# Performance work log

Hardware: AMD Instinct MI355X
Metric: run time of the kernel (lower is better)

Reference implementation:

```python
import jax, jax.numpy as jnp
import numpy as np

B, T, F, U = 64, 512, 1024, 64


def setup_inputs() -> dict:
    key = jax.random.key(0)
    ks = jax.random.split(key, 6)
    return {
        "x": jax.random.normal(ks[0], (B, T, F), dtype=jnp.float32),
        "kernel": jax.random.normal(ks[1], (F, U), dtype=jnp.float32) * (1.0 / np.sqrt(F)),
        "bias": jax.random.normal(ks[2], (U,), dtype=jnp.float32) * 0.02,
        "chain_kernel": jax.random.normal(ks[3], (U, U), dtype=jnp.float32) * 0.1,
        "left_boundary": jax.random.normal(ks[4], (U,), dtype=jnp.float32) * 0.1,
        "right_boundary": jax.random.normal(ks[5], (U,), dtype=jnp.float32) * 0.1,
    }


def _viterbi_decode(potentials, chain_kernel):
    # potentials: [B, T, U], chain_kernel: [U, U]
    def step(alpha, pot_t):
        # alpha: [B, U] best score ending in each tag at t-1
        scores = alpha[:, :, None] + chain_kernel[None, :, :] + pot_t[:, None, :]  # [B, U_prev, U_cur]
        return jnp.max(scores, axis=1), jnp.argmax(scores, axis=1)

    pots_t = jnp.moveaxis(potentials[:, 1:], 1, 0)  # [T-1, B, U]
    alpha_last, backptrs = jax.lax.scan(step, potentials[:, 0], pots_t)
    last_tag = jnp.argmax(alpha_last, axis=-1)  # [B]

    def back(tag, bp):
        prev = jnp.take_along_axis(bp, tag[:, None], axis=1)[:, 0]
        return prev, prev

    _, tags = jax.lax.scan(back, last_tag, backptrs, reverse=True)  # [T-1, B], positions 0..T-2
    path = jnp.concatenate([jnp.moveaxis(tags, 0, 1), last_tag[:, None]], axis=1)
    return path.astype(jnp.int32)


def reference(x, kernel, bias, chain_kernel, left_boundary, right_boundary):
    # dense projection (activation = linear)
    potentials = jnp.einsum("btf,fu->btu", x, kernel) + bias  # [B, T, U]
    # boundary energies (mask=None path: add to first/last timestep)
    potentials = potentials.at[:, 0, :].add(left_boundary)
    potentials = potentials.at[:, -1, :].add(right_boundary)
    return _viterbi_decode(potentials, chain_kernel)
```

## Files before the change

kernel.cpp:

```cpp
#include <hip/hip_runtime.h>

#define B_ 64
#define T_ 512
#define F_ 1024
#define U_ 64
#define FK 128
#define NCH (F_ / FK)

__device__ __forceinline__ void block_barrier_lds() {
    asm volatile("s_waitcnt lgkmcnt(0)" ::: "memory");
    __builtin_amdgcn_s_barrier();
    asm volatile("" ::: "memory");
}

__global__ __launch_bounds__(256, 2) void crf_gemm_kernel(
    const float* __restrict__ x, const float* __restrict__ w,
    const float* __restrict__ bias, const float* __restrict__ lb,
    const float* __restrict__ rb, float* __restrict__ pot)
{
    __shared__ float wlds[FK * U_];

    const int tid = threadIdx.x;
    const int rt = tid >> 4;
    const int ut = tid & 15;
    const int n0 = blockIdx.x * 64;
    const int r0 = rt * 4;
    const int u0 = ut * 4;

    float acc[4][4];
#pragma unroll
    for (int i = 0; i < 4; ++i)
#pragma unroll
        for (int j = 0; j < 4; ++j) acc[i][j] = 0.f;

    const float* xrow = x + (size_t)(n0 + r0) * F_;

    float4 wst[8];
#pragma unroll
    for (int l = 0; l < 8; ++l)
        wst[l] = *reinterpret_cast<const float4*>(w + (size_t)(l * 256 + tid) * 4);
#pragma unroll
    for (int l = 0; l < 8; ++l)
        *reinterpret_cast<float4*>(&wlds[(l * 256 + tid) * 4]) = wst[l];
    __syncthreads();

    float4 xp0[4], xp1[4];
#pragma unroll
    for (int i = 0; i < 4; ++i)
        xp0[i] = *reinterpret_cast<const float4*>(xrow + (size_t)i * F_ + 0);
#pragma unroll
    for (int i = 0; i < 4; ++i)
        xp1[i] = *reinterpret_cast<const float4*>(xrow + (size_t)i * F_ + 4);

    for (int c = 0; c < NCH; ++c) {
        if (c + 1 < NCH) {
#pragma unroll
            for (int l = 0; l < 8; ++l)
                wst[l] = *reinterpret_cast<const float4*>(
                    w + (size_t)(c + 1) * (FK * U_) + (size_t)(l * 256 + tid) * 4);
        }

        float4 wc[4];
#pragma unroll
        for (int j = 0; j < 4; ++j)
            wc[j] = *reinterpret_cast<const float4*>(&wlds[(0 + j) * U_ + u0]);

        for (int kk = 0; kk < FK / 4; ++kk) {
            const int kg = (c * FK + kk * 4 + 8) & (F_ - 1);
            float4 xn[4];
#pragma unroll
            for (int i = 0; i < 4; ++i)
                xn[i] = *reinterpret_cast<const float4*>(xrow + (size_t)i * F_ + kg);

            float4 wn[4];
            const int krn = (kk * 4 + 4) & (FK - 1);
#pragma unroll
            for (int j = 0; j < 4; ++j)
                wn[j] = *reinterpret_cast<const float4*>(&wlds[(krn + j) * U_ + u0]);

#pragma unroll
            for (int ff = 0; ff < 4; ++ff) {
                const float4 wf = wc[ff];
#pragma unroll
                for (int i = 0; i < 4; ++i) {
                    const float xs = (ff == 0) ? xp0[i].x : (ff == 1) ? xp0[i].y
                                   : (ff == 2) ? xp0[i].z : xp0[i].w;
                    acc[i][0] = fmaf(xs, wf.x, acc[i][0]);
                    acc[i][1] = fmaf(xs, wf.y, acc[i][1]);
                    acc[i][2] = fmaf(xs, wf.z, acc[i][2]);
                    acc[i][3] = fmaf(xs, wf.w, acc[i][3]);
                }
            }
#pragma unroll
            for (int i = 0; i < 4; ++i) { xp0[i] = xp1[i]; xp1[i] = xn[i]; }
#pragma unroll
            for (int j = 0; j < 4; ++j) wc[j] = wn[j];
        }

        if (c + 1 < NCH) {
            __syncthreads();
#pragma unroll
            for (int l = 0; l < 8; ++l)
                *reinterpret_cast<float4*>(&wlds[(l * 256 + tid) * 4]) = wst[l];
            __syncthreads();
        }
    }

    const int t0 = n0 & (T_ - 1);
    const float4 bs4 = *reinterpret_cast<const float4*>(bias + u0);
    const float4 lb4 = *reinterpret_cast<const float4*>(lb + u0);
    const float4 rb4 = *reinterpret_cast<const float4*>(rb + u0);

#pragma unroll
    for (int i = 0; i < 4; ++i) {
        const int n = n0 + r0 + i;
        const int t = t0 + r0 + i;
        float4 o;
        o.x = acc[i][0] + bs4.x;
        o.y = acc[i][1] + bs4.y;
        o.z = acc[i][2] + bs4.z;
        o.w = acc[i][3] + bs4.w;
        if (t == 0)      { o.x += lb4.x; o.y += lb4.y; o.z += lb4.z; o.w += lb4.w; }
        if (t == T_ - 1) { o.x += rb4.x; o.y += rb4.y; o.z += rb4.z; o.w += rb4.w; }
        *reinterpret_cast<float4*>(pot + (size_t)n * U_ + u0) = o;
    }
}

__global__ __launch_bounds__(256) void crf_viterbi_kernel(
    const float* __restrict__ pot, const float* __restrict__ chain,
    int* __restrict__ path)
{
    const int b = blockIdx.x;
    const int tid = threadIdx.x;
    const int u = tid & 63;
    const int g = tid >> 6;

    __shared__ __align__(16) float alpha_s[64];
    __shared__ float pval[4][64];
    __shared__ int   pidx[4][64];
    __shared__ unsigned char bp[T_ - 1][64];
    __shared__ unsigned char cmap[4][64];
    __shared__ int es[4];

    float chain_r[16];
#pragma unroll
    for (int k = 0; k < 16; ++k)
        chain_r[k] = chain[(size_t)(g * 16 + k) * U_ + u];

    const float* potb = pot + (size_t)b * T_ * U_;

    if (g == 0) alpha_s[u] = potb[u];

    float p0 = potb[1 * U_ + u];
    float p1 = potb[2 * U_ + u];
    float p2 = potb[3 * U_ + u];
    block_barrier_lds();

    for (int t = 1; t < T_; ++t) {
        const int tp = (t + 3 < T_) ? (t + 3) : (T_ - 1);
        const float pnew = potb[(size_t)tp * U_ + u];
        const float pc = p0;

        const float4* a4 = reinterpret_cast<const float4*>(alpha_s);
        float s[16];
#pragma unroll
        for (int q = 0; q < 4; ++q) {
            const float4 av = a4[g * 4 + q];
            s[q * 4 + 0] = (av.x + chain_r[q * 4 + 0]) + pc;
            s[q * 4 + 1] = (av.y + chain_r[q * 4 + 1]) + pc;
            s[q * 4 + 2] = (av.z + chain_r[q * 4 + 2]) + pc;
            s[q * 4 + 3] = (av.w + chain_r[q * 4 + 3]) + pc;
        }
        float tv[8]; int ti[8];
#pragma unroll
        for (int i = 0; i < 8; ++i) {
            const bool gt = s[2 * i + 1] > s[2 * i];
            tv[i] = gt ? s[2 * i + 1] : s[2 * i];
            ti[i] = gt ? 2 * i + 1 : 2 * i;
        }
        float uv[4]; int ui[4];
#pragma unroll
        for (int i = 0; i < 4; ++i) {
            const bool gt = tv[2 * i + 1] > tv[2 * i];
            uv[i] = gt ? tv[2 * i + 1] : tv[2 * i];
            ui[i] = gt ? ti[2 * i + 1] : ti[2 * i];
        }
        const bool g0_ = uv[1] > uv[0];
        const float w0 = g0_ ? uv[1] : uv[0];
        const int   i0 = g0_ ? ui[1] : ui[0];
        const bool g1_ = uv[3] > uv[2];
        const float w1 = g1_ ? uv[3] : uv[2];
        const int   i1 = g1_ ? ui[3] : ui[2];
        const bool gf = w1 > w0;
        const float bv16 = gf ? w1 : w0;
        const int   bi16 = gf ? i1 : i0;

        pval[g][u] = bv16;
        pidx[g][u] = g * 16 + bi16;
        block_barrier_lds();

        if (g == 0) {
            float bv = pval[0][u];
            int   bi = pidx[0][u];
#pragma unroll
            for (int j = 1; j < 4; ++j) {
                const float vv = pval[j][u];
                if (vv > bv) { bv = vv; bi = pidx[j][u]; }
            }
            alpha_s[u] = bv;
            bp[t - 1][u] = (unsigned char)bi;
        }
        block_barrier_lds();

        p0 = p1; p1 = p2; p2 = pnew;
    }

    const int r0c = g * 128;
    const int r1c = (g == 3) ? (T_ - 1) : (g + 1) * 128;

    {
        int tag = u;
        for (int r = r1c - 1; r >= r0c; --r) tag = bp[r][tag];
        cmap[g][u] = (unsigned char)tag;
    }
    block_barrier_lds();

    if (tid == 0) {
        float bvv = alpha_s[0];
        int bii = 0;
        for (int v = 1; v < 64; ++v) {
            const float a = alpha_s[v];
            if (a > bvv) { bvv = a; bii = v; }
        }
        path[(size_t)b * T_ + (T_ - 1)] = bii;
        const int e3 = bii;
        const int e2 = cmap[3][e3];
        const int e1 = cmap[2][e2];
        const int e0 = cmap[1][e1];
        es[0] = e0; es[1] = e1; es[2] = e2; es[3] = e3;
    }
    block_barrier_lds();

    if (u == 0) {
        int tag = es[g];
        int* pb = path + (size_t)b * T_;
        for (int r = r1c - 1; r >= r0c; --r) {
            tag = bp[r][tag];
            pb[r] = tag;
        }
    }
}

extern "C" void kernel_launch(void* const* d_in, const int* in_sizes, int n_in,
                              void* d_out, int out_size, void* d_ws, size_t ws_size,
                              hipStream_t stream) {
    const float* x  = (const float*)d_in[0];
    const float* w  = (const float*)d_in[1];
    const float* bs = (const float*)d_in[2];
    const float* ck = (const float*)d_in[3];
    const float* lb = (const float*)d_in[4];
    const float* rb = (const float*)d_in[5];

    float* pot = (float*)d_ws;
    int* path  = (int*)d_out;

    crf_gemm_kernel<<<dim3(B_ * T_ / 64), dim3(256), 0, stream>>>(x, w, bs, lb, rb, pot);
    crf_viterbi_kernel<<<dim3(B_), dim3(256), 0, stream>>>(pot, ck, path);
}
```

Baseline: 413.9 us.

## Halve GEMM row tile, raise occupancy, simplify Viterbi argmax and barriers

The GEMM kernel now gives each block 32 rows instead of 64, each thread 2 rows instead of 4, and launch bounds target 4 blocks per CU, doubling the grid. The goal is more parallelism and occupancy on the memory-bound projection, at the cost of reloading the weight matrix into LDS twice as often. The Viterbi kernel swaps its tree-reduction argmax for a sequential scan and its custom LDS barrier for __syncthreads, and prefetches one timestep ahead instead of three. That lengthens the serial dependency chain and exposes more global-load latency in the latency-bound recurrence.

```diff
diff --git a/kernel.cpp b/kernel.cpp
--- a/kernel.cpp
+++ b/kernel.cpp
@@ -7,13 +7,7 @@
 #define FK 128
 #define NCH (F_ / FK)
 
-__device__ __forceinline__ void block_barrier_lds() {
-    asm volatile("s_waitcnt lgkmcnt(0)" ::: "memory");
-    __builtin_amdgcn_s_barrier();
-    asm volatile("" ::: "memory");
-}
-
-__global__ __launch_bounds__(256, 2) void crf_gemm_kernel(
+__global__ __launch_bounds__(256, 4) void crf_gemm_kernel(
     const float* __restrict__ x, const float* __restrict__ w,
     const float* __restrict__ bias, const float* __restrict__ lb,
     const float* __restrict__ rb, float* __restrict__ pot)
@@ -23,13 +17,13 @@
     const int tid = threadIdx.x;
     const int rt = tid >> 4;
     const int ut = tid & 15;
-    const int n0 = blockIdx.x * 64;
-    const int r0 = rt * 4;
+    const int n0 = blockIdx.x * 32;
+    const int r0 = rt * 2;
     const int u0 = ut * 4;
 
-    float acc[4][4];
-#pragma unroll
-    for (int i = 0; i < 4; ++i)
+    float acc[2][4];
+#pragma unroll
+    for (int i = 0; i < 2; ++i)
 #pragma unroll
         for (int j = 0; j < 4; ++j) acc[i][j] = 0.f;
 
@@ -44,12 +38,12 @@
         *reinterpret_cast<float4*>(&wlds[(l * 256 + tid) * 4]) = wst[l];
     __syncthreads();
 
-    float4 xp0[4], xp1[4];
-#pragma unroll
-    for (int i = 0; i < 4; ++i)
+    float4 xp0[2], xp1[2];
+#pragma unroll
+    for (int i = 0; i < 2; ++i)
         xp0[i] = *reinterpret_cast<const float4*>(xrow + (size_t)i * F_ + 0);
 #pragma unroll
-    for (int i = 0; i < 4; ++i)
+    for (int i = 0; i < 2; ++i)
         xp1[i] = *reinterpret_cast<const float4*>(xrow + (size_t)i * F_ + 4);
 
     for (int c = 0; c < NCH; ++c) {
@@ -67,9 +61,9 @@
 
         for (int kk = 0; kk < FK / 4; ++kk) {
             const int kg = (c * FK + kk * 4 + 8) & (F_ - 1);
-            float4 xn[4];
-#pragma unroll
-            for (int i = 0; i < 4; ++i)
+            float4 xn[2];
+#pragma unroll
+            for (int i = 0; i < 2; ++i)
                 xn[i] = *reinterpret_cast<const float4*>(xrow + (size_t)i * F_ + kg);
 
             float4 wn[4];
@@ -82,7 +76,7 @@
             for (int ff = 0; ff < 4; ++ff) {
                 const float4 wf = wc[ff];
 #pragma unroll
-                for (int i = 0; i < 4; ++i) {
+                for (int i = 0; i < 2; ++i) {
                     const float xs = (ff == 0) ? xp0[i].x : (ff == 1) ? xp0[i].y
                                    : (ff == 2) ? xp0[i].z : xp0[i].w;
                     acc[i][0] = fmaf(xs, wf.x, acc[i][0]);
@@ -92,7 +86,7 @@
                 }
             }
 #pragma unroll
-            for (int i = 0; i < 4; ++i) { xp0[i] = xp1[i]; xp1[i] = xn[i]; }
+            for (int i = 0; i < 2; ++i) { xp0[i] = xp1[i]; xp1[i] = xn[i]; }
 #pragma unroll
             for (int j = 0; j < 4; ++j) wc[j] = wn[j];
         }
@@ -112,7 +106,7 @@
     const float4 rb4 = *reinterpret_cast<const float4*>(rb + u0);
 
 #pragma unroll
-    for (int i = 0; i < 4; ++i) {
+    for (int i = 0; i < 2; ++i) {
         const int n = n0 + r0 + i;
         const int t = t0 + r0 + i;
         float4 o;
@@ -150,69 +144,44 @@
     const float* potb = pot + (size_t)b * T_ * U_;
 
     if (g == 0) alpha_s[u] = potb[u];
-
-    float p0 = potb[1 * U_ + u];
-    float p1 = potb[2 * U_ + u];
-    float p2 = potb[3 * U_ + u];
-    block_barrier_lds();
+    __syncthreads();
+
+    float pc = potb[(size_t)U_ + u];
 
     for (int t = 1; t < T_; ++t) {
-        const int tp = (t + 3 < T_) ? (t + 3) : (T_ - 1);
-        const float pnew = potb[(size_t)tp * U_ + u];
-        const float pc = p0;
+        const int tn = (t + 1 < T_) ? (t + 1) : (T_ - 1);
+        const float pn = potb[(size_t)tn * U_ + u];
 
         const float4* a4 = reinterpret_cast<const float4*>(alpha_s);
-        float s[16];
+        float best = -3.402823466e38f;
+        int bidx = 0;
 #pragma unroll
         for (int q = 0; q < 4; ++q) {
             const float4 av = a4[g * 4 + q];
-            s[q * 4 + 0] = (av.x + chain_r[q * 4 + 0]) + pc;
-            s[q * 4 + 1] = (av.y + chain_r[q * 4 + 1]) + pc;
-            s[q * 4 + 2] = (av.z + chain_r[q * 4 + 2]) + pc;
-            s[q * 4 + 3] = (av.w + chain_r[q * 4 + 3]) + pc;
-        }
-        float tv[8]; int ti[8];
-#pragma unroll
-        for (int i = 0; i < 8; ++i) {
-            const bool gt = s[2 * i + 1] > s[2 * i];
-            tv[i] = gt ? s[2 * i + 1] : s[2 * i];
-            ti[i] = gt ? 2 * i + 1 : 2 * i;
-        }
-        float uv[4]; int ui[4];
-#pragma unroll
-        for (int i = 0; i < 4; ++i) {
-            const bool gt = tv[2 * i + 1] > tv[2 * i];
-            uv[i] = gt ? tv[2 * i + 1] : tv[2 * i];
-            ui[i] = gt ? ti[2 * i + 1] : ti[2 * i];
-        }
-        const bool g0_ = uv[1] > uv[0];
-        const float w0 = g0_ ? uv[1] : uv[0];
-        const int   i0 = g0_ ? ui[1] : ui[0];
-        const bool g1_ = uv[3] > uv[2];
-        const float w1 = g1_ ? uv[3] : uv[2];
-        const int   i1 = g1_ ? ui[3] : ui[2];
-        const bool gf = w1 > w0;
-        const float bv16 = gf ? w1 : w0;
-        const int   bi16 = gf ? i1 : i0;
-
-        pval[g][u] = bv16;
-        pidx[g][u] = g * 16 + bi16;
-        block_barrier_lds();
-
+            const float avv[4] = {av.x, av.y, av.z, av.w};
+#pragma unroll
+            for (int kk = 0; kk < 4; ++kk) {
+                const int k = q * 4 + kk;
+                const float s2 = (avv[kk] + chain_r[k]) + pc;
+                if (s2 > best) { best = s2; bidx = g * 16 + k; }
+            }
+        }
+        pval[g][u] = best;
+        pidx[g][u] = bidx;
+        __syncthreads();
         if (g == 0) {
             float bv = pval[0][u];
             int   bi = pidx[0][u];
 #pragma unroll
             for (int j = 1; j < 4; ++j) {
-                const float vv = pval[j][u];
-                if (vv > bv) { bv = vv; bi = pidx[j][u]; }
+                const float v = pval[j][u];
+                if (v > bv) { bv = v; bi = pidx[j][u]; }
             }
+            bp[t - 1][u] = (unsigned char)bi;
             alpha_s[u] = bv;
-            bp[t - 1][u] = (unsigned char)bi;
-        }
-        block_barrier_lds();
-
-        p0 = p1; p1 = p2; p2 = pnew;
+        }
+        __syncthreads();
+        pc = pn;
     }
 
     const int r0c = g * 128;
@@ -223,7 +192,7 @@
         for (int r = r1c - 1; r >= r0c; --r) tag = bp[r][tag];
         cmap[g][u] = (unsigned char)tag;
     }
-    block_barrier_lds();
+    __syncthreads();
 
     if (tid == 0) {
         float bvv = alpha_s[0];
@@ -239,7 +208,7 @@
         const int e0 = cmap[1][e1];
         es[0] = e0; es[1] = e1; es[2] = e2; es[3] = e3;
     }
-    block_barrier_lds();
+    __syncthreads();
 
     if (u == 0) {
         int tag = es[g];
@@ -264,6 +233,6 @@
     float* pot = (float*)d_ws;
     int* path  = (int*)d_out;
 
-    crf_gemm_kernel<<<dim3(B_ * T_ / 64), dim3(256), 0, stream>>>(x, w, bs, lb, rb, pot);
+    crf_gemm_kernel<<<dim3(B_ * T_ / 32), dim3(256), 0, stream>>>(x, w, bs, lb, rb, pot);
     crf_viterbi_kernel<<<dim3(B_), dim3(256), 0, stream>>>(pot, ck, path);
 }
```

After: 376.6 us. 1.1x faster.
